# Optimization experiments

Hardware: AMD Instinct MI355X
Metric: run time of the kernel (lower is better)

## Reference

```python
import jax, jax.numpy as jnp
import numpy as np

GRID_SIZE = 3
LN_EPS = 1e-5
BASIS_EPS = 1e-6


def setup_inputs() -> dict:
    key = jax.random.key(0)
    ks = jax.random.split(key, 5)
    B, S, D_IN, D_OUT, SE_H = 8, 1024, 1024, 1024, 32
    x = jax.random.normal(ks[0], (B, S, D_IN), dtype=jnp.float32)
    base_weight = jax.random.normal(ks[1], (D_OUT, D_IN), dtype=jnp.float32) * 0.01
    spline_weight = jax.random.normal(ks[2], (D_OUT, D_IN, GRID_SIZE), dtype=jnp.float32) * 0.005
    ln_w = jnp.ones((D_OUT,), dtype=jnp.float32)
    ln_b = jnp.zeros((D_OUT,), dtype=jnp.float32)
    se_w1 = jax.random.normal(ks[3], (SE_H, D_OUT), dtype=jnp.float32) * 0.03
    se_b1 = jnp.zeros((SE_H,), dtype=jnp.float32)
    se_w2 = jax.random.normal(ks[4], (D_OUT, SE_H), dtype=jnp.float32) * 0.03
    se_b2 = jnp.zeros((D_OUT,), dtype=jnp.float32)
    return {"x": x, "base_weight": base_weight, "spline_weight": spline_weight,
            "ln_w": ln_w, "ln_b": ln_b, "se_w1": se_w1, "se_b1": se_b1,
            "se_w2": se_w2, "se_b2": se_b2}


def _kan_layer(x2d, base_weight, spline_weight, ln_w, ln_b, se_w1, se_b1, se_w2, se_b2):
    # x2d: [N, D_in]
    base = x2d @ base_weight.T                                   # [N, D_out]
    grid = jnp.linspace(-1.0, 1.0, GRID_SIZE).astype(x2d.dtype)  # [G]
    dist = jnp.abs(x2d[..., None] - grid)                        # [N, D_in, G]
    basis = jnp.where(dist < 1.0, (1.0 - dist) ** 2, 0.0)
    basis = basis / (basis.sum(axis=-1, keepdims=True) + BASIS_EPS)
    spline = jnp.einsum('nig,oig->no', basis, spline_weight)     # [N, D_out]
    out = base + spline
    # LayerNorm (dropout is identity at inference)
    mu = out.mean(axis=-1, keepdims=True)
    var = ((out - mu) ** 2).mean(axis=-1, keepdims=True)
    out = (out - mu) * jax.lax.rsqrt(var + LN_EPS) * ln_w + ln_b
    # SE gating (2D branch: applied per flattened token)
    h = jnp.maximum(out @ se_w1.T + se_b1, 0.0)
    se = jax.nn.sigmoid(h @ se_w2.T + se_b2)
    return out * se


def reference(x, base_weight, spline_weight, ln_w, ln_b, se_w1, se_b1, se_w2, se_b2):
    B, S, D = x.shape
    out = _kan_layer(x.reshape(-1, D), base_weight, spline_weight,
                     ln_w, ln_b, se_w1, se_b1, se_w2, se_b2)
    return out.reshape(B, S, -1)
```

## Files before the change

### kernel.cpp

```cpp
#include <hip/hip_runtime.h>
#include <hip/hip_bf16.h>
#include <math.h>

typedef __attribute__((ext_vector_type(8))) __bf16 bf16x8;
typedef __attribute__((ext_vector_type(4))) float f32x4;

#define NTOK 8192
#define DIN 1024
#define DOUT 1024
#define KAUG 4096
#define SEH 32

#define BK 64
#define NKT (KAUG / BK)

static __device__ __forceinline__ unsigned short f2bf(float f) {
  union { float f; unsigned u; } v; v.f = f;
  unsigned r = (v.u + 0x7FFFu + ((v.u >> 16) & 1u)) >> 16;
  return (unsigned short)r;
}

__global__ __launch_bounds__(256) void prep(const float* __restrict__ x,
                                            const float* __restrict__ bw,
                                            const float* __restrict__ sw,
                                            const float* __restrict__ w1,
                                            const float* __restrict__ w2,
                                            ushort* __restrict__ Aaug,
                                            ushort* __restrict__ Waug,
                                            ushort* __restrict__ w1b,
                                            ushort* __restrict__ w2b) {
  const int b = blockIdx.x;
  if (b < 32768) {
    const int id = b * 256 + threadIdx.x;
    const float v = x[id];
    const float d0 = fabsf(v + 1.f), d1 = fabsf(v), d2 = fabsf(v - 1.f);
    float b0 = (d0 < 1.f) ? (1.f - d0) * (1.f - d0) : 0.f;
    float b1 = (d1 < 1.f) ? (1.f - d1) * (1.f - d1) : 0.f;
    float b2 = (d2 < 1.f) ? (1.f - d2) * (1.f - d2) : 0.f;
    const float inv = 1.f / (b0 + b1 + b2 + 1e-6f);
    ushort4 o;
    o.x = f2bf(v);
    o.y = f2bf(b0 * inv);
    o.z = f2bf(b1 * inv);
    o.w = f2bf(b2 * inv);
    ((ushort4*)Aaug)[id] = o;
  } else if (b < 32768 + 4096) {
    const int id = (b - 32768) * 256 + threadIdx.x;
    ushort4 o;
    o.x = f2bf(bw[id]);
    o.y = f2bf(sw[id * 3 + 0]);
    o.z = f2bf(sw[id * 3 + 1]);
    o.w = f2bf(sw[id * 3 + 2]);
    ((ushort4*)Waug)[id] = o;
  } else {
    const int id = (b - 32768 - 4096) * 256 + threadIdx.x;
    if (id < SEH * DOUT) w1b[id] = f2bf(w1[id]);
    else w2b[id - SEH * DOUT] = f2bf(w2[id - SEH * DOUT]);
  }
}

#define WAITVM(N) asm volatile("s_waitcnt vmcnt(" #N ")" ::: "memory")
#define SB0() __builtin_amdgcn_sched_barrier(0)

__global__ __launch_bounds__(256, 2) void gemm_ns(const ushort* __restrict__ A,
                                                  const ushort* __restrict__ B,
                                                  float* __restrict__ C) {
  __shared__ ushort As[2][128 * BK];
  __shared__ ushort Bs[2][128 * BK];
  const int tid = threadIdx.x;
  const int wid = tid >> 6, lane = tid & 63;
  const int l16 = lane & 15, lk = lane >> 4;
  const int wm = wid >> 1, wn = wid & 1;

  const int g = (blockIdx.x & 7) * 64 + (blockIdx.x >> 3);
  const int bm = g >> 3;
  const int bn = g & 7;

  const ushort* Ab = A + (size_t)bm * 128 * KAUG;
  const ushort* Bb = B + (size_t)bn * 128 * KAUG;

  const int lrow = lane >> 3;
  const int lcb = (lane & 7) ^ lrow;

  const int aBase = (wm * 64 + l16) * 64;
  const int bBase = (wn * 64 + l16) * 64;
  const int sw0 = ((l16 & 4) << 3) + ((lk ^ (l16 & 3)) << 3);
  const int sw1 = sw0 ^ 32;

  f32x4 acc[4][4] = {};

#define STAGE_A(kt, buf, r)                                                     \
  __builtin_amdgcn_global_load_lds(                                             \
      (const __attribute__((address_space(1))) void*)(Ab +                      \
          (size_t)((r) * 32 + wid * 8 + lrow) * KAUG + (kt) * BK + lcb * 8),    \
      (__attribute__((address_space(3))) void*)(&As[buf][((r) * 256 + wid * 64) * 8]), \
      16, 0, 0)
#define STAGE_B(kt, buf, r)                                                     \
  __builtin_amdgcn_global_load_lds(                                             \
      (const __attribute__((address_space(1))) void*)(Bb +                      \
          (size_t)((r) * 32 + wid * 8 + lrow) * KAUG + (kt) * BK + lcb * 8),    \
      (__attribute__((address_space(3))) void*)(&Bs[buf][((r) * 256 + wid * 64) * 8]), \
      16, 0, 0)
#define STAGE_ALL(kt, buf)                                                      \
  do {                                                                          \
    STAGE_A(kt, buf, 0); STAGE_A(kt, buf, 1); STAGE_A(kt, buf, 2); STAGE_A(kt, buf, 3); \
    STAGE_B(kt, buf, 0); STAGE_B(kt, buf, 1); STAGE_B(kt, buf, 2); STAGE_B(kt, buf, 3); \
  } while (0)

#define TILE(kt, CB, NB)                                                        \
  do {                                                                          \
    if ((kt) < NKT - 1) {                                                       \
      STAGE_ALL((kt) + 1, NB);                                                  \
      WAITVM(8);                                                                \
    } else {                                                                    \
      WAITVM(0);                                                                \
    }                                                                           \
    __builtin_amdgcn_s_barrier();                                               \
    SB0();                            \
    bf16x8 af[4][2], bfr[4][2];                                                 \
    _Pragma("unroll")                                                           \
    for (int m = 0; m < 4; ++m) {                                               \
      af[m][0] = *(const bf16x8*)&As[CB][aBase + m * 1024 + sw0];               \
      af[m][1] = *(const bf16x8*)&As[CB][aBase + m * 1024 + sw1];               \
    }                                                                           \
    _Pragma("unroll")                                                           \
    for (int n = 0; n < 4; ++n) {                                               \
      bfr[n][0] = *(const bf16x8*)&Bs[CB][bBase + n * 1024 + sw0];              \
      bfr[n][1] = *(const bf16x8*)&Bs[CB][bBase + n * 1024 + sw1];              \
    }                                                                           \
    __builtin_amdgcn_s_setprio(1);                                              \
    _Pragma("unroll")                                                           \
    for (int k2 = 0; k2 < 2; ++k2)                                              \
      _Pragma("unroll")                                                         \
      for (int m = 0; m < 4; ++m)                                               \
        _Pragma("unroll")                                                       \
        for (int n = 0; n < 4; ++n)                                             \
          acc[m][n] = __builtin_amdgcn_mfma_f32_16x16x32_bf16(                  \
              af[m][k2], bfr[n][k2], acc[m][n], 0, 0, 0);                       \
    __builtin_amdgcn_s_setprio(0);                                              \
    __builtin_amdgcn_s_barrier();                                               \
    SB0();         \
  } while (0)

  STAGE_ALL(0, 0);

  for (int kt2 = 0; kt2 < NKT; kt2 += 2) {
    TILE(kt2, 0, 1);
    TILE(kt2 + 1, 1, 0);
  }

  float* Cb = C + (size_t)(bm * 128 + wm * 64) * DOUT + bn * 128 + wn * 64;
#pragma unroll
  for (int m = 0; m < 4; ++m)
#pragma unroll
    for (int n = 0; n < 4; ++n)
#pragma unroll
      for (int j = 0; j < 4; ++j)
        Cb[(size_t)(m * 16 + lk * 4 + j) * DOUT + n * 16 + l16] = acc[m][n][j];
}

__global__ __launch_bounds__(256) void ln_se_mfma(
    float* __restrict__ out,
    const float* __restrict__ ln_w, const float* __restrict__ ln_b,
    const ushort* __restrict__ w1b, const float* __restrict__ se_b1,
    const ushort* __restrict__ w2b, const float* __restrict__ se_b2) {
  __shared__ float Yl[16 * 1028];
  __shared__ float Hpart[4][512];
  __shared__ unsigned Hb[256];
  const int tid = threadIdx.x;
  const int w = tid >> 6, lane = tid & 63;
  const int l16 = lane & 15, lk = lane >> 4;
  const int tok0 = blockIdx.x * 16;

  float4 lwv[4], lbv[4];
#pragma unroll
  for (int q = 0; q < 4; ++q) {
    lwv[q] = ((const float4*)ln_w)[q * 64 + lane];
    lbv[q] = ((const float4*)ln_b)[q * 64 + lane];
  }

  for (int qt = 0; qt < 4; ++qt) {
    const int tl = w * 4 + qt;
    const float4* r0 = (const float4*)(out + (size_t)(tok0 + tl) * DOUT);
    float4 v[4];
#pragma unroll
    for (int q = 0; q < 4; ++q) v[q] = r0[q * 64 + lane];
    float s = 0.f, ss = 0.f;
#pragma unroll
    for (int q = 0; q < 4; ++q) {
      s += v[q].x + v[q].y + v[q].z + v[q].w;
      ss += v[q].x * v[q].x + v[q].y * v[q].y + v[q].z * v[q].z + v[q].w * v[q].w;
    }
#pragma unroll
    for (int m = 32; m; m >>= 1) { s += __shfl_xor(s, m); ss += __shfl_xor(ss, m); }
    const float mu = s * (1.f / (float)DOUT);
    const float inv = rsqrtf(ss * (1.f / (float)DOUT) - mu * mu + 1e-5f);
#pragma unroll
    for (int q = 0; q < 4; ++q) {
      float4 yv;
      yv.x = (v[q].x - mu) * inv * lwv[q].x + lbv[q].x;
      yv.y = (v[q].y - mu) * inv * lwv[q].y + lbv[q].y;
      yv.z = (v[q].z - mu) * inv * lwv[q].z + lbv[q].z;
      yv.w = (v[q].w - mu) * inv * lwv[q].w + lbv[q].w;
      *(float4*)&Yl[tl * 1028 + (q * 64 + lane) * 4] = yv;
    }
  }
  __syncthreads();

  f32x4 acc1[2] = {};
#pragma unroll
  for (int s = 0; s < 8; ++s) {
    const int ks = w * 8 + s;
    const int k = ks * 32 + lk * 8;
    const float* yp = &Yl[l16 * 1028 + k];
    const f32x4 q0 = *(const f32x4*)yp;
    const f32x4 q1 = *(const f32x4*)(yp + 4);
    bf16x8 af;
    af[0] = (__bf16)q0[0]; af[1] = (__bf16)q0[1];
    af[2] = (__bf16)q0[2]; af[3] = (__bf16)q0[3];
    af[4] = (__bf16)q1[0]; af[5] = (__bf16)q1[1];
    af[6] = (__bf16)q1[2]; af[7] = (__bf16)q1[3];
#pragma unroll
    for (int nt = 0; nt < 2; ++nt) {
      const bf16x8 bf = *(const bf16x8*)(w1b + (nt * 16 + l16) * 1024 + ks * 32 + lk * 8);
      acc1[nt] = __builtin_amdgcn_mfma_f32_16x16x32_bf16(af, bf, acc1[nt], 0, 0, 0);
    }
  }
#pragma unroll
  for (int nt = 0; nt < 2; ++nt)
#pragma unroll
    for (int j = 0; j < 4; ++j)
      Hpart[w][(lk * 4 + j) * 32 + nt * 16 + l16] = acc1[nt][j];
  __syncthreads();

  {
    const int e2 = tid * 2;
    float h0 = Hpart[0][e2] + Hpart[1][e2] + Hpart[2][e2] + Hpart[3][e2];
    float h1 = Hpart[0][e2 + 1] + Hpart[1][e2 + 1] + Hpart[2][e2 + 1] + Hpart[3][e2 + 1];
    h0 = fmaxf(h0 + se_b1[e2 & 31], 0.f);
    h1 = fmaxf(h1 + se_b1[(e2 & 31) + 1], 0.f);
    Hb[tid] = (unsigned)f2bf(h0) | ((unsigned)f2bf(h1) << 16);
  }
  __syncthreads();

  union { uint4 u; bf16x8 v; } ha;
  ha.u = *(const uint4*)&Hb[l16 * 16 + lk * 4];
  const int nbase = w * 256;
#pragma unroll
  for (int nt = 0; nt < 16; ++nt) {
    const int col = nbase + nt * 16 + l16;
    const bf16x8 bf = *(const bf16x8*)(w2b + col * 32 + lk * 8);
    f32x4 gz = {0.f, 0.f, 0.f, 0.f};
    gz = __builtin_amdgcn_mfma_f32_16x16x32_bf16(ha.v, bf, gz, 0, 0, 0);
    const float b2 = se_b2[col];
#pragma unroll
    for (int j = 0; j < 4; ++j) {
      const int tl = lk * 4 + j;
      const float sg = 1.f / (1.f + __expf(-(gz[j] + b2)));
      out[(size_t)(tok0 + tl) * DOUT + col] = Yl[tl * 1028 + col] * sg;
    }
  }
}

extern "C" void kernel_launch(void* const* d_in, const int* in_sizes, int n_in,
                              void* d_out, int out_size, void* d_ws, size_t ws_size,
                              hipStream_t stream) {
  const float* x = (const float*)d_in[0];
  const float* bw = (const float*)d_in[1];
  const float* sw = (const float*)d_in[2];
  const float* ln_w = (const float*)d_in[3];
  const float* ln_b = (const float*)d_in[4];
  const float* se_w1 = (const float*)d_in[5];
  const float* se_b1 = (const float*)d_in[6];
  const float* se_w2 = (const float*)d_in[7];
  const float* se_b2 = (const float*)d_in[8];
  float* out = (float*)d_out;

  ushort* Aaug = (ushort*)d_ws;
  ushort* Waug = Aaug + (size_t)NTOK * KAUG;
  ushort* w1b = Waug + (size_t)DOUT * KAUG;
  ushort* w2b = w1b + SEH * DOUT;

  prep<<<32768 + 4096 + 256, 256, 0, stream>>>(x, bw, sw, se_w1, se_w2,
                                               Aaug, Waug, w1b, w2b);
  gemm_ns<<<512, 256, 0, stream>>>(Aaug, Waug, out);
  ln_se_mfma<<<NTOK / 16, 256, 0, stream>>>(out, ln_w, ln_b,
                                            w1b, se_b1, w2b, se_b2);
}
```

Measured before the change: 108.1 us.

## Split SE weights into hi/lo bf16, vectorize prep, simplify GEMM wait

The SE weights are split into high and low bf16 parts, and the two SE matmuls each run two MFMAs, one per part, to recover near-fp32 weight precision. The prep kernel now handles four x values per thread, with float4 loads and two uint4 stores, which reduces the block count. The GEMM pipeline now waits for vmcnt(0) on every tile instead of vmcnt(8). This removes overlap of the next tile's prefetch with the current compute in exchange for simpler ordering. The SE precision change adds MFMA work and extra weight loads.

```diff
diff --git a/kernel.cpp b/kernel.cpp
--- a/kernel.cpp
+++ b/kernel.cpp
@@ -28,34 +28,57 @@
                                             ushort* __restrict__ Aaug,
                                             ushort* __restrict__ Waug,
                                             ushort* __restrict__ w1b,
-                                            ushort* __restrict__ w2b) {
+                                            ushort* __restrict__ w1lo,
+                                            ushort* __restrict__ w2b,
+                                            ushort* __restrict__ w2lo) {
   const int b = blockIdx.x;
-  if (b < 32768) {
-    const int id = b * 256 + threadIdx.x;
-    const float v = x[id];
-    const float d0 = fabsf(v + 1.f), d1 = fabsf(v), d2 = fabsf(v - 1.f);
-    float b0 = (d0 < 1.f) ? (1.f - d0) * (1.f - d0) : 0.f;
-    float b1 = (d1 < 1.f) ? (1.f - d1) * (1.f - d1) : 0.f;
-    float b2 = (d2 < 1.f) ? (1.f - d2) * (1.f - d2) : 0.f;
-    const float inv = 1.f / (b0 + b1 + b2 + 1e-6f);
-    ushort4 o;
-    o.x = f2bf(v);
-    o.y = f2bf(b0 * inv);
-    o.z = f2bf(b1 * inv);
-    o.w = f2bf(b2 * inv);
-    ((ushort4*)Aaug)[id] = o;
-  } else if (b < 32768 + 4096) {
-    const int id = (b - 32768) * 256 + threadIdx.x;
+  if (b < 8192) {
+    const int id4 = b * 256 + threadIdx.x;
+    const float4 xv = ((const float4*)x)[id4];
+    unsigned q[8];
+    const float xs[4] = {xv.x, xv.y, xv.z, xv.w};
+#pragma unroll
+    for (int h = 0; h < 4; ++h) {
+      const float v = xs[h];
+      const float d0 = fabsf(v + 1.f), d1 = fabsf(v), d2 = fabsf(v - 1.f);
+      const float b0 = (d0 < 1.f) ? (1.f - d0) * (1.f - d0) : 0.f;
+      const float b1 = (d1 < 1.f) ? (1.f - d1) * (1.f - d1) : 0.f;
+      const float b2 = (d2 < 1.f) ? (1.f - d2) * (1.f - d2) : 0.f;
+      const float inv = 1.f / (b0 + b1 + b2 + 1e-6f);
+      q[h * 2 + 0] = (unsigned)f2bf(v) | ((unsigned)f2bf(b0 * inv) << 16);
+      q[h * 2 + 1] = (unsigned)f2bf(b1 * inv) | ((unsigned)f2bf(b2 * inv) << 16);
+    }
+    uint4* dst = (uint4*)(Aaug + (size_t)id4 * 16);
+    uint4 u0, u1;
+    u0.x = q[0]; u0.y = q[1]; u0.z = q[2]; u0.w = q[3];
+    u1.x = q[4]; u1.y = q[5]; u1.z = q[6]; u1.w = q[7];
+    dst[0] = u0;
+    dst[1] = u1;
+  } else if (b < 8192 + 4096) {
+    const int id = (b - 8192) * 256 + threadIdx.x;
     ushort4 o;
     o.x = f2bf(bw[id]);
-    o.y = f2bf(sw[id * 3 + 0]);
-    o.z = f2bf(sw[id * 3 + 1]);
-    o.w = f2bf(sw[id * 3 + 2]);
+    o.y = f2bf(sw[(size_t)id * 3 + 0]);
+    o.z = f2bf(sw[(size_t)id * 3 + 1]);
+    o.w = f2bf(sw[(size_t)id * 3 + 2]);
     ((ushort4*)Waug)[id] = o;
   } else {
-    const int id = (b - 32768 - 4096) * 256 + threadIdx.x;
-    if (id < SEH * DOUT) w1b[id] = f2bf(w1[id]);
-    else w2b[id - SEH * DOUT] = f2bf(w2[id - SEH * DOUT]);
+    const int id = (b - 8192 - 4096) * 256 + threadIdx.x;
+    const int plane = id >> 16;
+    const int e = id & 65535;
+    float srcv;
+    ushort* dst;
+    int off;
+    if (e < SEH * DOUT) { srcv = w1[e]; off = e; dst = plane ? w1lo : w1b; }
+    else { srcv = w2[e - SEH * DOUT]; off = e - SEH * DOUT; dst = plane ? w2lo : w2b; }
+    const unsigned short hi = f2bf(srcv);
+    if (!plane) {
+      dst[off] = hi;
+    } else {
+      union { unsigned u; float f; } hv;
+      hv.u = ((unsigned)hi) << 16;
+      dst[off] = f2bf(srcv - hv.f);
+    }
   }
 }
 
@@ -109,14 +132,11 @@
 
 #define TILE(kt, CB, NB)                                                        \
   do {                                                                          \
-    if ((kt) < NKT - 1) {                                                       \
-      STAGE_ALL((kt) + 1, NB);                                                  \
-      WAITVM(8);                                                                \
-    } else {                                                                    \
-      WAITVM(0);                                                                \
-    }                                                                           \
+    if ((kt) < NKT - 1) STAGE_ALL((kt) + 1, NB);                                \
+    SB0();                                                                      \
+    WAITVM(0);           \
     __builtin_amdgcn_s_barrier();                                               \
-    SB0();                            \
+    SB0();                              \
     bf16x8 af[4][2], bfr[4][2];                                                 \
     _Pragma("unroll")                                                           \
     for (int m = 0; m < 4; ++m) {                                               \
@@ -138,8 +158,9 @@
           acc[m][n] = __builtin_amdgcn_mfma_f32_16x16x32_bf16(                  \
               af[m][k2], bfr[n][k2], acc[m][n], 0, 0, 0);                       \
     __builtin_amdgcn_s_setprio(0);                                              \
+    SB0();                             \
     __builtin_amdgcn_s_barrier();                                               \
-    SB0();         \
+    SB0();                  \
   } while (0)
 
   STAGE_ALL(0, 0);
@@ -162,8 +183,10 @@
 __global__ __launch_bounds__(256) void ln_se_mfma(
     float* __restrict__ out,
     const float* __restrict__ ln_w, const float* __restrict__ ln_b,
-    const ushort* __restrict__ w1b, const float* __restrict__ se_b1,
-    const ushort* __restrict__ w2b, const float* __restrict__ se_b2) {
+    const ushort* __restrict__ w1b, const ushort* __restrict__ w1lo,
+    const float* __restrict__ se_b1,
+    const ushort* __restrict__ w2b, const ushort* __restrict__ w2lo,
+    const float* __restrict__ se_b2) {
   __shared__ float Yl[16 * 1028];
   __shared__ float Hpart[4][512];
   __shared__ unsigned Hb[256];
@@ -222,8 +245,11 @@
     af[6] = (__bf16)q1[2]; af[7] = (__bf16)q1[3];
 #pragma unroll
     for (int nt = 0; nt < 2; ++nt) {
-      const bf16x8 bf = *(const bf16x8*)(w1b + (nt * 16 + l16) * 1024 + ks * 32 + lk * 8);
-      acc1[nt] = __builtin_amdgcn_mfma_f32_16x16x32_bf16(af, bf, acc1[nt], 0, 0, 0);
+      const size_t woff = (size_t)(nt * 16 + l16) * 1024 + ks * 32 + lk * 8;
+      const bf16x8 bh = *(const bf16x8*)(w1b + woff);
+      const bf16x8 bl = *(const bf16x8*)(w1lo + woff);
+      acc1[nt] = __builtin_amdgcn_mfma_f32_16x16x32_bf16(af, bh, acc1[nt], 0, 0, 0);
+      acc1[nt] = __builtin_amdgcn_mfma_f32_16x16x32_bf16(af, bl, acc1[nt], 0, 0, 0);
     }
   }
 #pragma unroll
@@ -249,9 +275,12 @@
 #pragma unroll
   for (int nt = 0; nt < 16; ++nt) {
     const int col = nbase + nt * 16 + l16;
-    const bf16x8 bf = *(const bf16x8*)(w2b + col * 32 + lk * 8);
+    const size_t woff = (size_t)col * 32 + lk * 8;
+    const bf16x8 bh = *(const bf16x8*)(w2b + woff);
+    const bf16x8 bl = *(const bf16x8*)(w2lo + woff);
     f32x4 gz = {0.f, 0.f, 0.f, 0.f};
-    gz = __builtin_amdgcn_mfma_f32_16x16x32_bf16(ha.v, bf, gz, 0, 0, 0);
+    gz = __builtin_amdgcn_mfma_f32_16x16x32_bf16(ha.v, bh, gz, 0, 0, 0);
+    gz = __builtin_amdgcn_mfma_f32_16x16x32_bf16(ha.v, bl, gz, 0, 0, 0);
     const float b2 = se_b2[col];
 #pragma unroll
     for (int j = 0; j < 4; ++j) {
@@ -279,11 +308,13 @@
   ushort* Aaug = (ushort*)d_ws;
   ushort* Waug = Aaug + (size_t)NTOK * KAUG;
   ushort* w1b = Waug + (size_t)DOUT * KAUG;
-  ushort* w2b = w1b + SEH * DOUT;
-
-  prep<<<32768 + 4096 + 256, 256, 0, stream>>>(x, bw, sw, se_w1, se_w2,
-                                               Aaug, Waug, w1b, w2b);
+  ushort* w1lo = w1b + SEH * DOUT;
+  ushort* w2b = w1lo + SEH * DOUT;
+  ushort* w2lo = w2b + SEH * DOUT;
+
+  prep<<<8192 + 4096 + 512, 256, 0, stream>>>(x, bw, sw, se_w1, se_w2,
+                                              Aaug, Waug, w1b, w1lo, w2b, w2lo);
   gemm_ns<<<512, 256, 0, stream>>>(Aaug, Waug, out);
   ln_se_mfma<<<NTOK / 16, 256, 0, stream>>>(out, ln_w, ln_b,
-                                            w1b, se_b1, w2b, se_b2);
-}
+                                            w1b, w1lo, se_b1, w2b, w2lo, se_b2);
+}
```

Result: slower. 116.2 us (+7.5%).
